# Kernel tuning notes

Hardware: AMD Instinct MI355X
Metric: run time of the kernel (lower is better)

Reference implementation:

```python
import jax, jax.numpy as jnp
import numpy as np

B, S, D, H = 32, 512, 1024, 16
DH = D // H
EPS = 1e-5
NEG = -1e9


def layer_norm(x, g, b):
    mu = jnp.mean(x, axis=-1, keepdims=True)
    var = jnp.mean(jnp.square(x - mu), axis=-1, keepdims=True)
    return (x - mu) * jax.lax.rsqrt(var + EPS) * g + b


def setup_inputs() -> dict:
    key = jax.random.key(0)
    ks = jax.random.split(key, 12)
    s = 1.0 / np.sqrt(D)
    inp = {
        "qk": jax.random.normal(ks[0], (B, S, D), jnp.float32),
        "v": jax.random.normal(ks[1], (B, S, D), jnp.float32),
        "mask": jax.random.randint(ks[2], (B, S), 0, 2).astype(jnp.int32),
        "qk_ln_g": jnp.ones((D,), jnp.float32),
        "qk_ln_b": jnp.zeros((D,), jnp.float32),
        "v_ln_g": jnp.ones((D,), jnp.float32),
        "v_ln_b": jnp.zeros((D,), jnp.float32),
        "Wq": jax.random.normal(ks[3], (D, D), jnp.float32) * s,
        "bq": jnp.zeros((D,), jnp.float32),
        "Wk": jax.random.normal(ks[4], (D, D), jnp.float32) * s,
        "bk": jnp.zeros((D,), jnp.float32),
        "Wv": jax.random.normal(ks[5], (D, D), jnp.float32) * s,
        "bv": jnp.zeros((D,), jnp.float32),
        "Wo": jax.random.normal(ks[6], (D, D), jnp.float32) * s,
        "bo": jnp.zeros((D,), jnp.float32),
    }
    return inp


def reference(qk, v, mask, qk_ln_g, qk_ln_b, v_ln_g, v_ln_b,
              Wq, bq, Wk, bk, Wv, bv, Wo, bo):
    # dual pre-norm
    qk_n = layer_norm(qk, qk_ln_g, qk_ln_b)          # [B,S,D]
    v_n = layer_norm(v, v_ln_g, v_ln_b)              # [B,S,D]
    # projections -> [B,S,H,DH]
    q = (qk_n @ Wq + bq).reshape(B, S, H, DH)
    k = (qk_n @ Wk + bk).reshape(B, S, H, DH)
    vv = (v_n @ Wv + bv).reshape(B, S, H, DH)
    # attention scores with key-padding mask
    scores = jnp.einsum("bqhd,bkhd->bhqk", q, k) / np.sqrt(DH)
    scores = jnp.where(mask[:, None, None, :] == 0, NEG, scores)
    attn = jax.nn.softmax(scores, axis=-1)           # [B,H,Sq,Sk]
    ctx = jnp.einsum("bhqk,bkhd->bqhd", attn, vv).reshape(B, S, D)
    a = ctx @ Wo + bo                                # output projection
    # residual on the normalized v (dropout is identity at eval)
    return v_n + a
```

## Files before the change

kernel.cpp:

```cpp
#include <hip/hip_runtime.h>
#include <hip/hip_bf16.h>

typedef __bf16 bf16;
typedef __bf16 bf16x2 __attribute__((ext_vector_type(2)));
typedef __bf16 bf16x4 __attribute__((ext_vector_type(4)));
typedef __bf16 bf16x8 __attribute__((ext_vector_type(8)));
typedef float f32x4 __attribute__((ext_vector_type(4)));

#define B_ 32
#define S_ 512
#define D_ 1024
#define H_ 16
#define DH_ 64
#define M_ (B_*S_)

#if __has_builtin(__builtin_amdgcn_exp2f)
#define FEXP2 __builtin_amdgcn_exp2f
#else
#define FEXP2 exp2f
#endif

__device__ __forceinline__ void async16(const void* g, void* l) {
  __builtin_amdgcn_global_load_lds(
      (const __attribute__((address_space(1))) unsigned int*)g,
      (__attribute__((address_space(3))) unsigned int*)l, 16, 0, 0);
}

__global__ __launch_bounds__(256) void ln_bf16(
    const float* __restrict__ qk, const float* __restrict__ v,
    const float* __restrict__ g1, const float* __restrict__ b1,
    const float* __restrict__ g2, const float* __restrict__ b2,
    bf16* __restrict__ o1, bf16* __restrict__ o2)
{
  int row = blockIdx.x;
  const float* src; const float* g; const float* b; bf16* o; int r;
  if (row < M_) { src=qk; g=g1; b=b1; o=o1; r=row; }
  else          { src=v;  g=g2; b=b2; o=o2; r=row-M_; }
  int t = threadIdx.x;
  float4 x = ((const float4*)(src + (size_t)r*D_))[t];
  float s  = x.x+x.y+x.z+x.w;
  float ss = x.x*x.x + x.y*x.y + x.z*x.z + x.w*x.w;
  #pragma unroll
  for (int off=32; off>=1; off>>=1) {
    s  += __shfl_xor(s,  off, 64);
    ss += __shfl_xor(ss, off, 64);
  }
  __shared__ float red[8];
  int w = t>>6, l = t&63;
  if (l==0){ red[w]=s; red[4+w]=ss; }
  __syncthreads();
  s  = red[0]+red[1]+red[2]+red[3];
  ss = red[4]+red[5]+red[6]+red[7];
  float mu  = s*(1.f/D_);
  float var = ss*(1.f/D_) - mu*mu;
  float rs  = rsqrtf(var + 1e-5f);
  float4 gg = ((const float4*)g)[t];
  float4 bb = ((const float4*)b)[t];
  bf16x4 ov;
  ov[0] = (bf16)((x.x-mu)*rs*gg.x + bb.x);
  ov[1] = (bf16)((x.y-mu)*rs*gg.y + bb.y);
  ov[2] = (bf16)((x.z-mu)*rs*gg.z + bb.z);
  ov[3] = (bf16)((x.w-mu)*rs*gg.w + bb.w);
  ((bf16x4*)(o + (size_t)r*D_))[t] = ov;
}

__global__ void wtrans(const float* __restrict__ W0, const float* __restrict__ W1,
                       const float* __restrict__ W2, const float* __restrict__ W3,
                       bf16* __restrict__ o0, bf16* __restrict__ o1,
                       bf16* __restrict__ o2, bf16* __restrict__ o3)
{
  int z = blockIdx.z;
  const float* W = z==0?W0: z==1?W1: z==2?W2: W3;
  bf16* o        = z==0?o0: z==1?o1: z==2?o2: o3;
  __shared__ float tile[32][33];
  int n0 = blockIdx.x*32, k0 = blockIdx.y*32;
  int tx = threadIdx.x, ty = threadIdx.y;
  #pragma unroll
  for (int i=0;i<4;i++) tile[ty + i*8][tx] = W[(size_t)(k0+ty+i*8)*D_ + n0+tx];
  __syncthreads();
  #pragma unroll
  for (int i=0;i<4;i++) o[(size_t)(n0+ty+i*8)*D_ + k0+tx] = (bf16)tile[tx][ty+i*8];
}

template<int MODE>
__global__ __launch_bounds__(256) void gemm_bt(
    const bf16* __restrict__ A, const bf16* __restrict__ Bt,
    const float* __restrict__ bias0, const float* __restrict__ bias1,
    const bf16* __restrict__ res,
    bf16* __restrict__ out0, bf16* __restrict__ out1, float* __restrict__ outf)
{
  __shared__ bf16 A_sh[128*64];
  __shared__ bf16 B_sh[128*64];
  int t = threadIdx.x;
  int nwg  = gridDim.x * gridDim.y;
  int orig = blockIdx.y * gridDim.x + blockIdx.x;
  int qch  = nwg >> 3;
  int wg   = (orig & 7) * qch + (orig >> 3);
  int bx = wg % gridDim.x, by = wg / gridDim.x;
  int n0 = bx*128, m0 = by*128;
  int w = t>>6, l = t&63, lr = l&15, lg = (l>>4)&3;
  int wm = w>>1, wn = w&1;
  f32x4 acc[4][4];
  #pragma unroll
  for (int m=0;m<4;m++)
    #pragma unroll
    for (int n=0;n<4;n++) acc[m][n] = (f32x4){0.f,0.f,0.f,0.f};

  for (int kt=0; kt<16; ++kt) {
    const bf16* Ab = A  + (size_t)m0*D_ + kt*64;
    const bf16* Bb = Bt + (size_t)n0*D_ + kt*64;
    #pragma unroll
    for (int i=0;i<4;i++){
      int c = i*256 + t;
      int row = c>>3, slot = (c&7) ^ (row&7);
      async16(Ab + (size_t)row*D_ + slot*8, &A_sh[c*8]);
      async16(Bb + (size_t)row*D_ + slot*8, &B_sh[c*8]);
    }
    __syncthreads();
    bf16x8 af[4][2], bfr[4][2];
    #pragma unroll
    for (int m=0;m<4;m++){
      int row = wm*64 + m*16 + lr;
      #pragma unroll
      for (int kk=0;kk<2;kk++)
        af[m][kk] = *(const bf16x8*)&A_sh[row*64 + (((kk*4+lg)^(lr&7))*8)];
    }
    #pragma unroll
    for (int n=0;n<4;n++){
      int row = wn*64 + n*16 + lr;
      #pragma unroll
      for (int kk=0;kk<2;kk++)
        bfr[n][kk] = *(const bf16x8*)&B_sh[row*64 + (((kk*4+lg)^(lr&7))*8)];
    }
    #pragma unroll
    for (int kk=0;kk<2;kk++)
      #pragma unroll
      for (int m=0;m<4;m++)
        #pragma unroll
        for (int n=0;n<4;n++)
          acc[m][n] = __builtin_amdgcn_mfma_f32_16x16x32_bf16(af[m][kk], bfr[n][kk], acc[m][n], 0,0,0);
    __syncthreads();
  }

  if (MODE == 0) {
    #pragma unroll
    for (int n=0;n<4;n++){
      int col = n0 + wn*64 + n*16 + lr;
      bf16* dst; int c;
      if (col < D_) { dst = out0; c = col; } else { dst = out1; c = col - D_; }
      float bv = (col < D_) ? bias0[c] : bias1[c];
      #pragma unroll
      for (int m=0;m<4;m++){
        #pragma unroll
        for (int j=0;j<4;j++){
          size_t row = (size_t)m0 + wm*64 + m*16 + lg*4 + j;
          dst[row*D_ + c] = (bf16)(acc[m][n][j] + bv);
        }
      }
    }
  } else if (MODE == 1) {
    #pragma unroll
    for (int n=0;n<4;n++){
      int col = n0 + wn*64 + n*16 + lr;
      int h = col >> 6, dh = col & 63;
      float bv = bias0[col];
      #pragma unroll
      for (int m=0;m<4;m++){
        int row = m0 + wm*64 + m*16 + lg*4;
        int b = row >> 9, s = row & 511;
        bf16x4 pk;
        #pragma unroll
        for (int j=0;j<4;j++) pk[j] = (bf16)(acc[m][n][j] + bv);
        *(bf16x4*)&out0[((size_t)(b*H_ + h)*DH_ + dh)*S_ + s] = pk;
      }
    }
  } else {
    #pragma unroll
    for (int m=0;m<4;m++){
      #pragma unroll
      for (int j=0;j<4;j++){
        size_t row = (size_t)m0 + wm*64 + m*16 + lg*4 + j;
        #pragma unroll
        for (int n=0;n<4;n++){
          int col = n0 + wn*64 + n*16 + lr;
          size_t idx = row*D_ + col;
          outf[idx] = acc[m][n][j] + bias0[col] + (float)res[idx];
        }
      }
    }
  }
}

__global__ __launch_bounds__(256) void attn_fwd(
    const bf16* __restrict__ Q, const bf16* __restrict__ K,
    const bf16* __restrict__ VT, const int* __restrict__ mask,
    bf16* __restrict__ ctx)
{
  int flat = blockIdx.x + (blockIdx.y<<2) + (blockIdx.z<<6);
  int work = (flat & 7)*256 + (flat >> 3);
  int qt = work & 3, h = (work>>2) & 15, b = work >> 6;
  int q0 = qt*128;
  int t = threadIdx.x, w = t>>6, l = t&63, lr = l&15, lg = (l>>4)&3;

  __shared__ bf16 Q_sh[8192];
  __shared__ bf16 K_s0[4096], K_s1[4096];
  __shared__ bf16 V_s0[4096], V_s1[4096];
  __shared__ float msk[512];

  const float SC = 0.125f * 1.44269504f;
  for (int i=t;i<512;i+=256) msk[i] = mask[b*S_+i] ? 0.f : -1.44269504e9f;

  size_t qbase  = ((size_t)(b*S_ + q0)*H_ + h)*DH_;
  size_t vtbase = (size_t)(b*H_ + h)*DH_*S_;

  #pragma unroll
  for (int i=0;i<4;i++){
    int c = i*256 + t;
    int clr=c&15, clg=(c>>4)&3, ckk=(c>>6)&1, q16=c>>7;
    async16(Q + qbase + (size_t)(q16*16+clr)*D_ + ckk*32 + clg*8, &Q_sh[c*8]);
  }
  {
    size_t kb = ((size_t)(b*S_)*H_ + h)*DH_;
    #pragma unroll
    for (int i=0;i<2;i++){
      int c = i*256 + t;
      int clr=c&15, clg=(c>>4)&3, ckk=(c>>6)&1, n16=c>>7;
      async16(K + kb + (size_t)(n16*16+clr)*D_ + ckk*32 + clg*8, &K_s0[c*8]);
      async16(VT + vtbase + (size_t)(n16*16+clr)*S_ + ckk*32 + clg*8, &V_s0[c*8]);
    }
  }
  __syncthreads();

  bf16x8 qa[2][2];
  #pragma unroll
  for (int s=0;s<2;s++)
    #pragma unroll
    for (int kk=0;kk<2;kk++)
      qa[s][kk] = *(const bf16x8*)&Q_sh[((((s*4+w)*2+kk)*4+lg)*16+lr)*8];

  f32x4 cacc[2][4];
  #pragma unroll
  for (int s=0;s<2;s++)
    #pragma unroll
    for (int n=0;n<4;n++) cacc[s][n] = (f32x4){0.f,0.f,0.f,0.f};
  float mrun[2] = {-3.0e38f, -3.0e38f};
  float lrun[2] = {0.f, 0.f};

  union UPA { unsigned u[4]; bf16x8 v; };
  UPA pa[2][2];

  for (int kt=0; kt<8; ++kt) {
    const bf16* Ks = (kt&1) ? K_s1 : K_s0;
    const bf16* Vs = (kt&1) ? V_s1 : V_s0;
    if (kt < 7) {
      bf16* Kd = (kt&1) ? K_s0 : K_s1;
      bf16* Vd = (kt&1) ? V_s0 : V_s1;
      size_t kb = ((size_t)(b*S_ + (kt+1)*64)*H_ + h)*DH_;
      size_t vb = vtbase + (kt+1)*64;
      #pragma unroll
      for (int i=0;i<2;i++){
        int c = i*256 + t;
        int clr=c&15, clg=(c>>4)&3, ckk=(c>>6)&1, n16=c>>7;
        async16(K + kb + (size_t)(n16*16+clr)*D_ + ckk*32 + clg*8, &Kd[c*8]);
        async16(VT + vb + (size_t)(n16*16+clr)*S_ + ckk*32 + clg*8, &Vd[c*8]);
      }
    }

    bf16x8 kf[4][2];
    #pragma unroll
    for (int n=0;n<4;n++)
      #pragma unroll
      for (int kk=0;kk<2;kk++)
        kf[n][kk] = *(const bf16x8*)&Ks[(((n*2+kk)*4+lg)*16+lr)*8];

    #pragma unroll
    for (int s=0;s<2;s++){
      float p[4][4];
      #pragma unroll
      for (int n=0;n<4;n++){
        f32x4 sa = (f32x4){0.f,0.f,0.f,0.f};
        #pragma unroll
        for (int kk=0;kk<2;kk++)
          sa = __builtin_amdgcn_mfma_f32_16x16x32_bf16(kf[n][kk], qa[s][kk], sa, 0,0,0);
        float4 mk = *(const float4*)&msk[kt*64 + n*16 + lg*4];
        p[n][0] = sa[0]*SC + mk.x;
        p[n][1] = sa[1]*SC + mk.y;
        p[n][2] = sa[2]*SC + mk.z;
        p[n][3] = sa[3]*SC + mk.w;
      }

      float pm = fmaxf(fmaxf(p[0][0],p[0][1]),fmaxf(p[0][2],p[0][3]));
      #pragma unroll
      for (int n=1;n<4;n++)
        pm = fmaxf(pm, fmaxf(fmaxf(p[n][0],p[n][1]),fmaxf(p[n][2],p[n][3])));
      pm = fmaxf(pm, __shfl_xor(pm, 16, 64));
      pm = fmaxf(pm, __shfl_xor(pm, 32, 64));

      if (__any((int)(pm - mrun[s] > 8.f))) {
        float mnew  = fmaxf(mrun[s], pm);
        float alpha = FEXP2(mrun[s] - mnew);
        mrun[s] = mnew;
        lrun[s] *= alpha;
        #pragma unroll
        for (int n=0;n<4;n++) cacc[s][n] *= alpha;
      }
      float ps = 0.f;
      #pragma unroll
      for (int n=0;n<4;n++)
        #pragma unroll
        for (int j=0;j<4;j++){ p[n][j] = FEXP2(p[n][j] - mrun[s]); ps += p[n][j]; }
      ps += __shfl_xor(ps, 16, 64);
      ps += __shfl_xor(ps, 32, 64);
      lrun[s] += ps;

      unsigned pk[4][2];
      #pragma unroll
      for (int n=0;n<4;n++)
        #pragma unroll
        for (int i=0;i<2;i++){
          union { bf16x2 v; unsigned u; } u2;
          u2.v[0] = (bf16)p[n][2*i];
          u2.v[1] = (bf16)p[n][2*i+1];
          pk[n][i] = u2.u;
        }
      int srcbase = (l&15) + ((l&16)<<1);
      #pragma unroll
      for (int w4=0; w4<4; ++w4){
        int src = srcbase + ((w4&2)<<3);
        unsigned lo0 = __shfl(pk[0][w4&1], src, 64);
        unsigned hi0 = __shfl(pk[1][w4&1], src, 64);
        unsigned lo1 = __shfl(pk[2][w4&1], src, 64);
        unsigned hi1 = __shfl(pk[3][w4&1], src, 64);
        pa[s][0].u[w4] = (l&32) ? hi0 : lo0;
        pa[s][1].u[w4] = (l&32) ? hi1 : lo1;
      }
    }

    #pragma unroll
    for (int nd=0;nd<4;nd++){
      bf16x8 vb0 = *(const bf16x8*)&Vs[(((nd*2+0)*4+lg)*16+lr)*8];
      bf16x8 vb1 = *(const bf16x8*)&Vs[(((nd*2+1)*4+lg)*16+lr)*8];
      #pragma unroll
      for (int s=0;s<2;s++){
        cacc[s][nd] = __builtin_amdgcn_mfma_f32_16x16x32_bf16(vb0, pa[s][0].v, cacc[s][nd], 0,0,0);
        cacc[s][nd] = __builtin_amdgcn_mfma_f32_16x16x32_bf16(vb1, pa[s][1].v, cacc[s][nd], 0,0,0);
      }
    }
    __syncthreads();
  }

  #pragma unroll
  for (int s=0;s<2;s++){
    float rl = 1.0f / lrun[s];
    size_t obase = qbase + (size_t)(s*64 + w*16 + lr)*D_;
    #pragma unroll
    for (int nd=0;nd<4;nd++){
      bf16x4 o4;
      #pragma unroll
      for (int j=0;j<4;j++) o4[j] = (bf16)(cacc[s][nd][j]*rl);
      *(bf16x4*)&ctx[obase + nd*16 + lg*4] = o4;
    }
  }
}

extern "C" void kernel_launch(void* const* d_in, const int* in_sizes, int n_in,
                              void* d_out, int out_size, void* d_ws, size_t ws_size,
                              hipStream_t stream)
{
  (void)in_sizes; (void)n_in; (void)out_size; (void)ws_size;
  const float* qk   = (const float*)d_in[0];
  const float* v    = (const float*)d_in[1];
  const int*   mask = (const int*)  d_in[2];
  const float* qk_g = (const float*)d_in[3];
  const float* qk_b = (const float*)d_in[4];
  const float* v_g  = (const float*)d_in[5];
  const float* v_b  = (const float*)d_in[6];
  const float* Wq   = (const float*)d_in[7];
  const float* bq   = (const float*)d_in[8];
  const float* Wk   = (const float*)d_in[9];
  const float* bk   = (const float*)d_in[10];
  const float* Wv   = (const float*)d_in[11];
  const float* bv   = (const float*)d_in[12];
  const float* Wo   = (const float*)d_in[13];
  const float* bo   = (const float*)d_in[14];
  float* out = (float*)d_out;

  char* ws = (char*)d_ws;
  size_t off = 0;
  auto alloc = [&](size_t bytes){ void* p = ws + off; off += (bytes + 255) & ~(size_t)255; return p; };
  bf16* qkn  = (bf16*)alloc((size_t)M_*D_*2);
  bf16* vn   = (bf16*)alloc((size_t)M_*D_*2);
  bf16* Qb   = (bf16*)alloc((size_t)M_*D_*2);
  bf16* Kb   = (bf16*)alloc((size_t)M_*D_*2);
  bf16* VTb  = (bf16*)alloc((size_t)M_*D_*2);
  bf16* Cb   = (bf16*)alloc((size_t)M_*D_*2);
  bf16* WqkT = (bf16*)alloc((size_t)2*D_*D_*2);
  bf16* WvT  = (bf16*)alloc((size_t)D_*D_*2);
  bf16* WoT  = (bf16*)alloc((size_t)D_*D_*2);

  ln_bf16<<<2*M_, 256, 0, stream>>>(qk, v, qk_g, qk_b, v_g, v_b, qkn, vn);
  wtrans<<<dim3(32,32,4), dim3(32,8), 0, stream>>>(Wq, Wk, Wv, Wo,
      WqkT, WqkT + (size_t)D_*D_, WvT, WoT);
  gemm_bt<0><<<dim3(16,128), 256, 0, stream>>>(qkn, WqkT, bq, bk, nullptr, Qb, Kb, nullptr);
  gemm_bt<1><<<dim3(8,128),  256, 0, stream>>>(vn,  WvT,  bv, nullptr, nullptr, VTb, nullptr, nullptr);
  attn_fwd<<<dim3(4, 16, 32), 256, 0, stream>>>(Qb, Kb, VTb, mask, Cb);
  gemm_bt<2><<<dim3(8,128),  256, 0, stream>>>(Cb, WoT, bo, nullptr, vn, nullptr, nullptr, out);
}
```

Before: 297.5 us.

## Double-buffer GEMM tiles and triple-buffer attention K/V with explicit waitcnt barriers

After: 279.7 us. 6.0% less time.

```diff
diff --git a/kernel.cpp b/kernel.cpp
--- a/kernel.cpp
+++ b/kernel.cpp
@@ -89,8 +89,8 @@
     const bf16* __restrict__ res,
     bf16* __restrict__ out0, bf16* __restrict__ out1, float* __restrict__ outf)
 {
-  __shared__ bf16 A_sh[128*64];
-  __shared__ bf16 B_sh[128*64];
+  __shared__ bf16 A_sh[2][128*64];
+  __shared__ bf16 B_sh[2][128*64];
   int t = threadIdx.x;
   int nwg  = gridDim.x * gridDim.y;
   int orig = blockIdx.y * gridDim.x + blockIdx.x;
@@ -100,38 +100,52 @@
   int n0 = bx*128, m0 = by*128;
   int w = t>>6, l = t&63, lr = l&15, lg = (l>>4)&3;
   int wm = w>>1, wn = w&1;
-  f32x4 acc[4][4];
-  #pragma unroll
-  for (int m=0;m<4;m++)
-    #pragma unroll
-    for (int n=0;n<4;n++) acc[m][n] = (f32x4){0.f,0.f,0.f,0.f};
-
-  for (int kt=0; kt<16; ++kt) {
+
+  auto stage = [&](int buf, int kt){
     const bf16* Ab = A  + (size_t)m0*D_ + kt*64;
     const bf16* Bb = Bt + (size_t)n0*D_ + kt*64;
     #pragma unroll
     for (int i=0;i<4;i++){
       int c = i*256 + t;
       int row = c>>3, slot = (c&7) ^ (row&7);
-      async16(Ab + (size_t)row*D_ + slot*8, &A_sh[c*8]);
-      async16(Bb + (size_t)row*D_ + slot*8, &B_sh[c*8]);
-    }
-    __syncthreads();
+      async16(Ab + (size_t)row*D_ + slot*8, &A_sh[buf][c*8]);
+      async16(Bb + (size_t)row*D_ + slot*8, &B_sh[buf][c*8]);
+    }
+  };
+
+  f32x4 acc[4][4];
+  #pragma unroll
+  for (int m=0;m<4;m++)
+    #pragma unroll
+    for (int n=0;n<4;n++) acc[m][n] = (f32x4){0.f,0.f,0.f,0.f};
+
+  stage(0, 0);
+  stage(1, 1);
+  asm volatile("s_waitcnt vmcnt(8)" ::: "memory");
+  __builtin_amdgcn_s_barrier();
+
+  for (int kt=0; kt<16; ++kt) {
+    int cur = kt & 1;
     bf16x8 af[4][2], bfr[4][2];
     #pragma unroll
     for (int m=0;m<4;m++){
       int row = wm*64 + m*16 + lr;
       #pragma unroll
       for (int kk=0;kk<2;kk++)
-        af[m][kk] = *(const bf16x8*)&A_sh[row*64 + (((kk*4+lg)^(lr&7))*8)];
+        af[m][kk] = *(const bf16x8*)&A_sh[cur][row*64 + (((kk*4+lg)^(lr&7))*8)];
     }
     #pragma unroll
     for (int n=0;n<4;n++){
       int row = wn*64 + n*16 + lr;
       #pragma unroll
       for (int kk=0;kk<2;kk++)
-        bfr[n][kk] = *(const bf16x8*)&B_sh[row*64 + (((kk*4+lg)^(lr&7))*8)];
-    }
+        bfr[n][kk] = *(const bf16x8*)&B_sh[cur][row*64 + (((kk*4+lg)^(lr&7))*8)];
+    }
+    asm volatile("s_waitcnt lgkmcnt(0)" ::: "memory");
+    __builtin_amdgcn_sched_barrier(0);
+    __builtin_amdgcn_s_barrier();
+    if (kt+2 < 16) stage(cur, kt+2);
+    __builtin_amdgcn_s_setprio(1);
     #pragma unroll
     for (int kk=0;kk<2;kk++)
       #pragma unroll
@@ -139,7 +153,10 @@
         #pragma unroll
         for (int n=0;n<4;n++)
           acc[m][n] = __builtin_amdgcn_mfma_f32_16x16x32_bf16(af[m][kk], bfr[n][kk], acc[m][n], 0,0,0);
-    __syncthreads();
+    __builtin_amdgcn_s_setprio(0);
+    if (kt < 14)       asm volatile("s_waitcnt vmcnt(8)" ::: "memory");
+    else if (kt == 14) asm volatile("s_waitcnt vmcnt(0)" ::: "memory");
+    if (kt < 15) { __builtin_amdgcn_sched_barrier(0); __builtin_amdgcn_s_barrier(); }
   }
 
   if (MODE == 0) {
@@ -202,9 +219,8 @@
   int q0 = qt*128;
   int t = threadIdx.x, w = t>>6, l = t&63, lr = l&15, lg = (l>>4)&3;
 
-  __shared__ bf16 Q_sh[8192];
-  __shared__ bf16 K_s0[4096], K_s1[4096];
-  __shared__ bf16 V_s0[4096], V_s1[4096];
+  __shared__ bf16 K_s[3][4096];
+  __shared__ bf16 V_s[3][4096];
   __shared__ float msk[512];
 
   const float SC = 0.125f * 1.44269504f;
@@ -213,30 +229,29 @@
   size_t qbase  = ((size_t)(b*S_ + q0)*H_ + h)*DH_;
   size_t vtbase = (size_t)(b*H_ + h)*DH_*S_;
 
-  #pragma unroll
-  for (int i=0;i<4;i++){
-    int c = i*256 + t;
-    int clr=c&15, clg=(c>>4)&3, ckk=(c>>6)&1, q16=c>>7;
-    async16(Q + qbase + (size_t)(q16*16+clr)*D_ + ckk*32 + clg*8, &Q_sh[c*8]);
-  }
-  {
-    size_t kb = ((size_t)(b*S_)*H_ + h)*DH_;
+  auto stageKV = [&](int slot, int kt){
+    size_t kb = ((size_t)(b*S_ + kt*64)*H_ + h)*DH_;
+    size_t vb = vtbase + kt*64;
     #pragma unroll
     for (int i=0;i<2;i++){
       int c = i*256 + t;
       int clr=c&15, clg=(c>>4)&3, ckk=(c>>6)&1, n16=c>>7;
-      async16(K + kb + (size_t)(n16*16+clr)*D_ + ckk*32 + clg*8, &K_s0[c*8]);
-      async16(VT + vtbase + (size_t)(n16*16+clr)*S_ + ckk*32 + clg*8, &V_s0[c*8]);
-    }
-  }
-  __syncthreads();
+      async16(K + kb + (size_t)(n16*16+clr)*D_ + ckk*32 + clg*8, &K_s[slot][c*8]);
+      async16(VT + vb + (size_t)(n16*16+clr)*S_ + ckk*32 + clg*8, &V_s[slot][c*8]);
+    }
+  };
 
   bf16x8 qa[2][2];
   #pragma unroll
   for (int s=0;s<2;s++)
     #pragma unroll
     for (int kk=0;kk<2;kk++)
-      qa[s][kk] = *(const bf16x8*)&Q_sh[((((s*4+w)*2+kk)*4+lg)*16+lr)*8];
+      qa[s][kk] = *(const bf16x8*)(Q + qbase + (size_t)(s*64 + w*16 + lr)*D_ + kk*32 + lg*8);
+
+  stageKV(0, 0);
+  stageKV(1, 1);
+  asm volatile("s_waitcnt vmcnt(4) lgkmcnt(0)" ::: "memory");
+  __builtin_amdgcn_s_barrier();
 
   f32x4 cacc[2][4];
   #pragma unroll
@@ -250,21 +265,9 @@
   UPA pa[2][2];
 
   for (int kt=0; kt<8; ++kt) {
-    const bf16* Ks = (kt&1) ? K_s1 : K_s0;
-    const bf16* Vs = (kt&1) ? V_s1 : V_s0;
-    if (kt < 7) {
-      bf16* Kd = (kt&1) ? K_s0 : K_s1;
-      bf16* Vd = (kt&1) ? V_s0 : V_s1;
-      size_t kb = ((size_t)(b*S_ + (kt+1)*64)*H_ + h)*DH_;
-      size_t vb = vtbase + (kt+1)*64;
-      #pragma unroll
-      for (int i=0;i<2;i++){
-        int c = i*256 + t;
-        int clr=c&15, clg=(c>>4)&3, ckk=(c>>6)&1, n16=c>>7;
-        async16(K + kb + (size_t)(n16*16+clr)*D_ + ckk*32 + clg*8, &Kd[c*8]);
-        async16(VT + vb + (size_t)(n16*16+clr)*S_ + ckk*32 + clg*8, &Vd[c*8]);
-      }
-    }
+    const bf16* Ks = K_s[kt%3];
+    const bf16* Vs = V_s[kt%3];
+    if (kt+2 < 8) stageKV((kt+2)%3, kt+2);
 
     bf16x8 kf[4][2];
     #pragma unroll
@@ -346,7 +349,11 @@
         cacc[s][nd] = __builtin_amdgcn_mfma_f32_16x16x32_bf16(vb1, pa[s][1].v, cacc[s][nd], 0,0,0);
       }
     }
-    __syncthreads();
+
+    asm volatile("s_waitcnt lgkmcnt(0)" ::: "memory");
+    if (kt < 6)       asm volatile("s_waitcnt vmcnt(4)" ::: "memory");
+    else if (kt == 6) asm volatile("s_waitcnt vmcnt(0)" ::: "memory");
+    if (kt < 7) { __builtin_amdgcn_sched_barrier(0); __builtin_amdgcn_s_barrier(); }
   }
 
   #pragma unroll
```
